# Kernel tuning notes

Hardware: AMD Instinct MI355X
Metric: run time of the kernel (lower is better)

The kernel has to match this reference:

```python
import jax, jax.numpy as jnp
import numpy as np

NUM_HEADS = 8
SCALE = 25.0
SIM_THRESH = 0.75


def setup_inputs() -> dict:
    key = jax.random.key(0)
    k1, k2, k3, k4 = jax.random.split(key, 4)
    B, N, C = 1, 2048, 1024
    x_cls = jax.random.normal(k1, (B, N, C), jnp.float32)
    cls_score = jax.random.uniform(k2, (N,), jnp.float32)
    fg_score = jax.random.uniform(k3, (N,), jnp.float32)
    W_qkv = jax.random.normal(k4, (3 * C, C), jnp.float32) * 0.02
    return {"x_cls": x_cls, "cls_score": cls_score, "fg_score": fg_score, "W_qkv": W_qkv}


def reference(x_cls, cls_score, fg_score, W_qkv):
    B, N, C = x_cls.shape
    H = NUM_HEADS
    hd = C // H
    # qkv projection (Linear without bias): [B,N,3C] -> [3,B,H,N,hd]
    qkv = (x_cls @ W_qkv.T).reshape(B, N, 3, H, hd).transpose(2, 0, 3, 1, 4)
    q, k, v = qkv[0], qkv[1], qkv[2]
    # cosine normalization
    qn = q / jnp.linalg.norm(q, axis=-1, keepdims=True)
    kn = k / jnp.linalg.norm(k, axis=-1, keepdims=True)
    vn = v / jnp.linalg.norm(v, axis=-1, keepdims=True)
    # cls_score broadcast to [1,1,1,N] (columns); fg_score is unused downstream
    cs = cls_score.reshape(1, 1, 1, N)
    # raw v-v similarity map [B,H,N,N]
    attn_cls_raw = vn @ jnp.swapaxes(vn, -2, -1)
    # use_mask=True path: mask[i,j] = cls_score[j] > cls_score[i] - 0.1
    cs_mask = (cs > jnp.swapaxes(cs, -2, -1) - 0.1).astype(x_cls.dtype)
    # scaled, score-weighted, masked attention; dropout p=0 is identity
    attn = jax.nn.softmax((qn @ jnp.swapaxes(kn, -2, -1)) * SCALE * cs * cs_mask, axis=-1)
    x = jnp.swapaxes(attn @ v, 1, 2).reshape(B, N, C)
    x_ori = jnp.swapaxes(v, 1, 2).reshape(B, N, C)
    x_out = jnp.concatenate([x, x_ori], axis=-1)  # [B,N,2C]
    # ave=True branch: head-averaged similarity + second softmax, masked renorm
    sim_raw = attn_cls_raw.sum(axis=1)[0] / H  # [N,N]
    sim_mask = (sim_raw > SIM_THRESH).astype(x_cls.dtype)
    sim_attn = attn.sum(axis=1)[0] / H
    sim_round2 = jax.nn.softmax(sim_attn, axis=-1)
    masked = sim_mask * sim_round2
    sim_round2 = masked / jnp.sum(masked, axis=-1, keepdims=True)
    return (x_out, sim_round2)
```

## Files before the change

kernel.cpp:

```cpp
#include <hip/hip_runtime.h>
#include <cstdint>

typedef unsigned short u16;
typedef __attribute__((ext_vector_type(8))) short short8;
typedef __attribute__((ext_vector_type(4))) short short4v;
typedef __attribute__((ext_vector_type(4))) float f32x4;

#define NTOK 2048
#define CDIM 1024
#define C3   3072
#define NH   8
#define HD   128

__device__ __forceinline__ float bf2f(u16 u) {
    return __uint_as_float(((unsigned)u) << 16);
}
__device__ __forceinline__ u16 f2bf(float f) {
    unsigned u = __float_as_uint(f);
    u += 0x7fffu + ((u >> 16) & 1u);
    return (u16)(u >> 16);
}
__device__ __forceinline__ void gld_lds16(const u16* g, u16* l) {
    __builtin_amdgcn_global_load_lds(
        (__attribute__((address_space(1))) void*)(u16*)g,
        (__attribute__((address_space(3))) void*)l, 16, 0, 0);
}

__global__ __launch_bounds__(256) void k_cast(const float* __restrict__ x,
                                              const float* __restrict__ w,
                                              u16* __restrict__ xb,
                                              u16* __restrict__ wb) {
    int t = blockIdx.x * blockDim.x + threadIdx.x;
    int stride = gridDim.x * blockDim.x;
    for (int i = t; i < (NTOK * CDIM) / 4; i += stride) {
        float4 v = ((const float4*)x)[i];
        ushort4 o;
        o.x = f2bf(v.x); o.y = f2bf(v.y); o.z = f2bf(v.z); o.w = f2bf(v.w);
        ((ushort4*)xb)[i] = o;
    }
    for (int i = t; i < (C3 * CDIM) / 4; i += stride) {
        float4 v = ((const float4*)w)[i];
        ushort4 o;
        o.x = f2bf(v.x); o.y = f2bf(v.y); o.z = f2bf(v.z); o.w = f2bf(v.w);
        ((ushort4*)wb)[i] = o;
    }
}

__global__ __launch_bounds__(256) void k_qkvn(const u16* __restrict__ A,
                                              const u16* __restrict__ B,
                                              u16* __restrict__ Qn,
                                              u16* __restrict__ Kn,
                                              u16* __restrict__ Vn,
                                              u16* __restrict__ Vt,
                                              float* __restrict__ out) {
    __shared__ u16 SB[2][16384];
    __shared__ float rowssq[128][2];
    u16* T = (u16*)SB;
    const int tid = threadIdx.x;
    const int lane = tid & 63;
    const int wid = tid >> 6;
    const int wm = wid >> 1, wn = wid & 1;
    const int q = lane >> 4, l16 = lane & 15;
    const int s = blockIdx.x;
    const int which = s >> 3, h = s & 7;
    const int m0 = blockIdx.y * 128, n0 = s * 128;

    const u16* aP[4];
    const u16* bP[4];
#pragma unroll
    for (int t = 0; t < 4; t++) {
        int sl = tid + t * 256;
        int r = sl >> 3, c = (sl & 7) * 8;
        aP[t] = &A[(long long)(m0 + r) * CDIM + c];
        bP[t] = &B[(long long)(n0 + r) * CDIM + c];
    }
#pragma unroll
    for (int t = 0; t < 4; t++) {
        int sl = tid + t * 256;
        gld_lds16(aP[t], &SB[0][sl * 8]);
        gld_lds16(bP[t], &SB[0][8192 + sl * 8]);
        aP[t] += 64;
        bP[t] += 64;
    }

    f32x4 zero4 = {0.f, 0.f, 0.f, 0.f};
    f32x4 acc[4][4];
#pragma unroll
    for (int i = 0; i < 4; i++)
#pragma unroll
        for (int j = 0; j < 4; j++) acc[i][j] = zero4;

    for (int jt = 0; jt < 16; ++jt) {
        const u16* As = SB[jt & 1];
        const u16* Bs = SB[jt & 1] + 8192;
        asm volatile("s_waitcnt vmcnt(0)" ::: "memory");
        __builtin_amdgcn_s_barrier();
        asm volatile("" ::: "memory");
        if (jt < 15) {
            u16* Sx = SB[(jt + 1) & 1];
#pragma unroll
            for (int t = 0; t < 4; t++) {
                int sl = tid + t * 256;
                gld_lds16(aP[t], &Sx[sl * 8]);
                gld_lds16(bP[t], &Sx[8192 + sl * 8]);
                aP[t] += 64;
                bP[t] += 64;
            }
        }
#pragma unroll
        for (int ks = 0; ks < 2; ks++) {
            short8 af[4], bfr[4];
#pragma unroll
            for (int tm = 0; tm < 4; tm++)
                af[tm] = *(const short8*)&As[(wm * 64 + tm * 16 + l16) * 64 + ks * 32 + q * 8];
#pragma unroll
            for (int tn = 0; tn < 4; tn++)
                bfr[tn] = *(const short8*)&Bs[(wn * 64 + tn * 16 + l16) * 64 + ks * 32 + q * 8];
#pragma unroll
            for (int tm = 0; tm < 4; tm++)
#pragma unroll
                for (int tn = 0; tn < 4; tn++)
                    acc[tm][tn] = __builtin_amdgcn_mfma_f32_16x16x32_bf16(
                        af[tm], bfr[tn], acc[tm][tn], 0, 0, 0);
        }
    }

    __syncthreads();
#pragma unroll
    for (int tm = 0; tm < 4; tm++)
#pragma unroll
        for (int r = 0; r < 4; r++) {
            float p = 0.f;
#pragma unroll
            for (int tn = 0; tn < 4; tn++) p += acc[tm][tn][r] * acc[tm][tn][r];
            p += __shfl_xor(p, 1);
            p += __shfl_xor(p, 2);
            p += __shfl_xor(p, 4);
            p += __shfl_xor(p, 8);
            if (l16 == 0) rowssq[wm * 64 + tm * 16 + q * 4 + r][wn] = p;
        }
    __syncthreads();
    float rinv[4][4];
#pragma unroll
    for (int tm = 0; tm < 4; tm++)
#pragma unroll
        for (int r = 0; r < 4; r++) {
            int rl = wm * 64 + tm * 16 + q * 4 + r;
            rinv[tm][r] = rsqrtf(rowssq[rl][0] + rowssq[rl][1]);
        }
    u16* dstBase = (which == 0 ? Qn : which == 1 ? Kn : Vn);
#pragma unroll
    for (int tm = 0; tm < 4; tm++)
#pragma unroll
        for (int tn = 0; tn < 4; tn++)
#pragma unroll
            for (int r = 0; r < 4; r++) {
                int rl = wm * 64 + tm * 16 + q * 4 + r;
                int d = wn * 64 + tn * 16 + l16;
                dstBase[(long long)(m0 + rl) * CDIM + h * HD + d] =
                    f2bf(acc[tm][tn][r] * rinv[tm][r]);
            }
    if (which == 2) {
#pragma unroll
        for (int tm = 0; tm < 4; tm++)
#pragma unroll
            for (int tn = 0; tn < 4; tn++)
#pragma unroll
                for (int r = 0; r < 4; r++) {
                    int rl = wm * 64 + tm * 16 + q * 4 + r;
                    int d = wn * 64 + tn * 16 + l16;
                    float v = acc[tm][tn][r];
                    out[(long long)(m0 + rl) * 2048 + 1024 + h * HD + d] = v;
                    T[rl * 136 + d] = f2bf(v);
                }
        __syncthreads();
#pragma unroll
        for (int p = 0; p < 2; p++) {
            int drow = p * 64 + (tid >> 2);
            int nc = (tid & 3) * 32;
            u16 buf[32];
#pragma unroll
            for (int i = 0; i < 32; i++) buf[i] = T[(nc + i) * 136 + drow];
            u16* dst = &Vt[(long long)(h * HD + drow) * NTOK + m0 + nc];
            *(short8*)&dst[0] = *(short8*)&buf[0];
            *(short8*)&dst[8] = *(short8*)&buf[8];
            *(short8*)&dst[16] = *(short8*)&buf[16];
            *(short8*)&dst[24] = *(short8*)&buf[24];
        }
    }
}

__global__ __launch_bounds__(256) void k_gemm_mask(const u16* __restrict__ A,
                                                   const u16* __restrict__ B,
                                                   unsigned char* __restrict__ Cv,
                                                   int K, int lda, int ldb, int ldc,
                                                   float scale) {
    __shared__ u16 As2[2][8192];
    __shared__ u16 Bs2[2][4096];
    __shared__ __attribute__((aligned(16))) unsigned char Tm[128][80];
    const int tid = threadIdx.x;
    const int lane = tid & 63;
    const int wid = tid >> 6;
    const int wm = wid >> 1, wn = wid & 1;
    const int q = lane >> 4, l16 = lane & 15;
    const int bid = blockIdx.x + 32 * blockIdx.y;
    const int sw = (bid & 7) * 64 + (bid >> 3);
    const int m0 = (sw >> 5) * 128, n0 = (sw & 31) * 64;

    const u16* aP[4];
    const u16* bP[2];
#pragma unroll
    for (int t = 0; t < 4; t++) {
        int s = tid + t * 256;
        aP[t] = &A[(long long)(m0 + (s >> 3)) * lda + (s & 7) * 8];
    }
#pragma unroll
    for (int t = 0; t < 2; t++) {
        int s = tid + t * 256;
        bP[t] = &B[(long long)(n0 + (s >> 3)) * ldb + (s & 7) * 8];
    }
#pragma unroll
    for (int t = 0; t < 4; t++) { gld_lds16(aP[t], &As2[0][(tid + t * 256) * 8]); aP[t] += 64; }
#pragma unroll
    for (int t = 0; t < 2; t++) { gld_lds16(bP[t], &Bs2[0][(tid + t * 256) * 8]); bP[t] += 64; }

    f32x4 zero4 = {0.f, 0.f, 0.f, 0.f};
    f32x4 acc[4][2];
#pragma unroll
    for (int i = 0; i < 4; i++)
#pragma unroll
        for (int j = 0; j < 2; j++) acc[i][j] = zero4;

    const int NIT = K / 64;
    for (int jt = 0; jt < NIT; ++jt) {
        const u16* As = As2[jt & 1];
        const u16* Bs = Bs2[jt & 1];
        asm volatile("s_waitcnt vmcnt(0)" ::: "memory");
        __builtin_amdgcn_s_barrier();
        asm volatile("" ::: "memory");
        if (jt < NIT - 1) {
            u16* Ax = As2[(jt + 1) & 1];
            u16* Bx = Bs2[(jt + 1) & 1];
#pragma unroll
            for (int t = 0; t < 4; t++) { gld_lds16(aP[t], &Ax[(tid + t * 256) * 8]); aP[t] += 64; }
#pragma unroll
            for (int t = 0; t < 2; t++) { gld_lds16(bP[t], &Bx[(tid + t * 256) * 8]); bP[t] += 64; }
        }
#pragma unroll
        for (int ks = 0; ks < 2; ks++) {
            short8 af[4], bfr[2];
#pragma unroll
            for (int tm = 0; tm < 4; tm++)
                af[tm] = *(const short8*)&As[(wm * 64 + tm * 16 + l16) * 64 + ks * 32 + q * 8];
#pragma unroll
            for (int tn = 0; tn < 2; tn++)
                bfr[tn] = *(const short8*)&Bs[(wn * 32 + tn * 16 + l16) * 64 + ks * 32 + q * 8];
#pragma unroll
            for (int tm = 0; tm < 4; tm++)
#pragma unroll
                for (int tn = 0; tn < 2; tn++)
                    acc[tm][tn] = __builtin_amdgcn_mfma_f32_16x16x32_bf16(
                        af[tm], bfr[tn], acc[tm][tn], 0, 0, 0);
        }
    }

#pragma unroll
    for (int tm = 0; tm < 4; tm++)
#pragma unroll
        for (int tn = 0; tn < 2; tn++) {
            int col = wn * 32 + tn * 16 + l16;
            int rowbase = wm * 64 + tm * 16 + q * 4;
#pragma unroll
            for (int r = 0; r < 4; r++)
                Tm[rowbase + r][col] = (acc[tm][tn][r] * scale > 0.75f) ? 1 : 0;
        }
    __syncthreads();
    {
        int row = tid >> 1, half = (tid & 1) * 32;
        const short8* sm = (const short8*)&Tm[row][half];
        short8* dm = (short8*)&Cv[(long long)(m0 + row) * ldc + n0 + half];
        dm[0] = sm[0]; dm[1] = sm[1];
    }
}

__global__ __launch_bounds__(256, 2) void k_attn9(const u16* __restrict__ Qn,
                                                  const u16* __restrict__ Kn,
                                                  const u16* __restrict__ Vt,
                                                  const float* __restrict__ cls,
                                                  u16* __restrict__ P,
                                                  float* __restrict__ Spart,
                                                  u16* __restrict__ Xpart) {
    __shared__ u16 Kf[2][8192];
    __shared__ u16 Vf[2][8192];
    __shared__ u16 Et[8192];
    const int bid = blockIdx.x + 16 * (blockIdx.y + 4 * blockIdx.z);
    const int sw = (bid & 7) * 64 + (bid >> 3);
    const int h = sw >> 6;
    const int jc = (sw >> 4) & 3;
    const int i0 = (sw & 15) * 128;
    const int jbase = jc * 512;
    const int tid = threadIdx.x, lane = tid & 63, wid = tid >> 6;
    const int q = lane >> 4, l16 = lane & 15;
    const int wm = wid >> 1, wn = wid & 1;

    short8 af[4][4];
#pragma unroll
    for (int m = 0; m < 4; m++)
#pragma unroll
        for (int kt = 0; kt < 4; kt++)
            af[m][kt] = *(const short8*)&Qn[(long long)(i0 + wm * 64 + m * 16 + l16) * CDIM +
                                            h * HD + kt * 32 + q * 8];
    float cls_i[4][4];
#pragma unroll
    for (int m = 0; m < 4; m++)
#pragma unroll
        for (int r = 0; r < 4; r++)
            cls_i[m][r] = cls[i0 + wm * 64 + m * 16 + q * 4 + r] - 0.1f;

    const u16* ksrc[4];
    const u16* vsrc[4];
#pragma unroll
    for (int t = 0; t < 4; t++) {
        int g = wid * 4 + t;
        int tn = g >> 2, kt = g & 3;
        ksrc[t] = &Kn[(long long)(jbase + tn * 16 + l16) * CDIM + h * HD + kt * 32 + q * 8];
        int n = g >> 1, ks = g & 1;
        vsrc[t] = &Vt[(long long)(h * HD + n * 16 + l16) * NTOK + jbase + (ks * 4 + q) * 8];
    }

    f32x4 zero4 = {0.f, 0.f, 0.f, 0.f};
    f32x4 pv[4][4];
#pragma unroll
    for (int m = 0; m < 4; m++)
#pragma unroll
        for (int n = 0; n < 4; n++) pv[m][n] = zero4;
    float sums[4][4];
#pragma unroll
    for (int m = 0; m < 4; m++)
#pragma unroll
        for (int r = 0; r < 4; r++) sums[m][r] = 0.f;

#pragma unroll
    for (int t = 0; t < 4; t++) {
        int g = wid * 4 + t;
        gld_lds16(ksrc[t], &Kf[0][(g * 64 + lane) * 8]);
        gld_lds16(vsrc[t], &Vf[0][(g * 64 + lane) * 8]);
        ksrc[t] += 64 * CDIM;
        vsrc[t] += 64;
    }

    for (int jt = 0; jt < 8; ++jt) {
        const int j0 = jbase + jt * 64;
        const int cur = jt & 1;
        u16* Kc = Kf[cur];
        if (jt == 0)
            asm volatile("s_waitcnt vmcnt(0)" ::: "memory");
        else
            asm volatile("s_waitcnt vmcnt(4)" ::: "memory");
        float cjv[2];
        cjv[0] = cls[j0 + (wn * 2 + 0) * 16 + l16];
        cjv[1] = cls[j0 + (wn * 2 + 1) * 16 + l16];
        asm volatile("" ::: "memory");
        __builtin_amdgcn_s_barrier();
        asm volatile("" ::: "memory");
        if (jt < 7) {
            u16* Kx = Kf[cur ^ 1];
            u16* Vx = Vf[cur ^ 1];
#pragma unroll
            for (int t = 0; t < 4; t++) {
                int g = wid * 4 + t;
                gld_lds16(ksrc[t], &Kx[(g * 64 + lane) * 8]);
                gld_lds16(vsrc[t], &Vx[(g * 64 + lane) * 8]);
                ksrc[t] += 64 * CDIM;
                vsrc[t] += 64;
            }
        }
#pragma unroll
        for (int tn = 0; tn < 2; tn++) {
            int tng = wn * 2 + tn;
            short8 bfr[4];
#pragma unroll
            for (int kt = 0; kt < 4; kt++)
                bfr[kt] = *(const short8*)&Kc[((tng * 4 + kt) * 64 + lane) * 8];
            float cj = cjv[tn];
            float sc = 25.f * cj;
#pragma unroll
            for (int m = 0; m < 4; m++) {
                f32x4 acc = zero4;
                __builtin_amdgcn_s_setprio(1);
#pragma unroll
                for (int kt = 0; kt < 4; kt++)
                    acc = __builtin_amdgcn_mfma_f32_16x16x32_bf16(af[m][kt], bfr[kt],
                                                                  acc, 0, 0, 0);
                __builtin_amdgcn_s_setprio(0);
                int ibase = wm * 64 + m * 16 + q * 4;
#pragma unroll
                for (int r = 0; r < 4; r++) {
                    float arg = (cj > cls_i[m][r]) ? acc[r] * sc : 0.f;
                    float e = __expf(arg);
                    sums[m][r] += e;
                    int il = ibase + r;
                    int jl = tng * 16 + l16;
                    Et[il * 64 + ((((jl >> 3) ^ (il & 7)) << 3) | (jl & 7))] = f2bf(e);
                }
            }
        }
        asm volatile("s_waitcnt lgkmcnt(0)" ::: "memory");
        __builtin_amdgcn_s_barrier();
        asm volatile("" ::: "memory");
        {
#pragma unroll
            for (int k = 0; k < 4; k++) {
                int il = k * 32 + (tid >> 3);
                int c = tid & 7;
                short8 ev = *(const short8*)&Et[il * 64 + ((c ^ (il & 7)) << 3)];
                *(short8*)&P[((long long)(h * NTOK + i0 + il)) * NTOK + j0 + c * 8] = ev;
            }
        }
        __builtin_amdgcn_s_setprio(1);
#pragma unroll
        for (int ks = 0; ks < 2; ks++) {
            short8 a2[4];
#pragma unroll
            for (int m2 = 0; m2 < 4; m2++) {
                int il = wm * 64 + m2 * 16 + l16;
                int ch = ks * 4 + q;
                a2[m2] = *(const short8*)&Et[il * 64 + ((ch ^ (il & 7)) << 3)];
            }
#pragma unroll
            for (int n2 = 0; n2 < 4; n2++) {
                short8 b2 = *(const short8*)&Vf[cur][(((wn * 4 + n2) * 2 + ks) * 64 + lane) * 8];
#pragma unroll
                for (int m2 = 0; m2 < 4; m2++)
                    pv[m2][n2] = __builtin_amdgcn_mfma_f32_16x16x32_bf16(
                        a2[m2], b2, pv[m2][n2], 0, 0, 0);
            }
        }
        __builtin_amdgcn_s_setprio(0);
    }
#pragma unroll
    for (int m = 0; m < 4; m++)
#pragma unroll
        for (int r = 0; r < 4; r++) {
            float s = sums[m][r];
            s += __shfl_xor(s, 1);
            s += __shfl_xor(s, 2);
            s += __shfl_xor(s, 4);
            s += __shfl_xor(s, 8);
            if (l16 == 0)
                Spart[((wn * 4 + jc) * NH + h) * NTOK + i0 + wm * 64 + m * 16 + q * 4 + r] = s;
        }
    u16* Xp = Xpart + (long long)jc * NTOK * CDIM;
#pragma unroll
    for (int m2 = 0; m2 < 4; m2++)
#pragma unroll
        for (int n2 = 0; n2 < 4; n2++)
#pragma unroll
            for (int r = 0; r < 4; r++) {
                int i = i0 + wm * 64 + m2 * 16 + q * 4 + r;
                int d = wn * 64 + n2 * 16 + l16;
                Xp[(long long)i * CDIM + h * HD + d] = f2bf(pv[m2][n2][r]);
            }
}

__global__ __launch_bounds__(256) void k_epi(const u16* __restrict__ Xpart,
                                             const float* __restrict__ Spart,
                                             const u16* __restrict__ P,
                                             const unsigned char* __restrict__ mask,
                                             float* __restrict__ out,
                                             float* __restrict__ out2) {
    __shared__ float redw[4];
    __shared__ float sArr[NH];
    const int i = blockIdx.x;
    const int t = threadIdx.x;
    const int lane = t & 63, w4 = t >> 6;
    if (t < NH) {
        float s = 0.f;
#pragma unroll
        for (int g = 0; g < 8; g++) s += Spart[(g * NH + t) * NTOK + i];
        sArr[t] = s;
    }
    __syncthreads();
    {
        int c = t * 4;
        int h = c >> 7;
        float acc[4] = {0.f, 0.f, 0.f, 0.f};
#pragma unroll
        for (int jc = 0; jc < 4; jc++) {
            short4v v = *(const short4v*)&Xpart[(long long)jc * NTOK * CDIM +
                                                (long long)i * CDIM + c];
#pragma unroll
            for (int k = 0; k < 4; k++) acc[k] += bf2f((u16)v[k]);
        }
        float invs = 1.f / sArr[h];
        float4 o;
        o.x = acc[0] * invs; o.y = acc[1] * invs; o.z = acc[2] * invs; o.w = acc[3] * invs;
        *(float4*)&out[(long long)i * 2048 + c] = o;
    }
    float invS[NH];
#pragma unroll
    for (int h = 0; h < NH; h++) invS[h] = 1.f / (8.f * sArr[h]);
    const int c0 = t * 8;
    float a[8] = {0.f, 0.f, 0.f, 0.f, 0.f, 0.f, 0.f, 0.f};
#pragma unroll
    for (int h = 0; h < NH; h++) {
        short8 p = *(const short8*)&P[((long long)h * NTOK + i) * NTOK + c0];
#pragma unroll
        for (int k = 0; k < 8; k++) a[k] += bf2f((u16)p[k]) * invS[h];
    }
    uint2 mv = *(const uint2*)(mask + (long long)i * NTOK + c0);
    unsigned char mk[8];
#pragma unroll
    for (int k = 0; k < 4; k++) {
        mk[k] = (unsigned char)((mv.x >> (8 * k)) & 0xffu);
        mk[k + 4] = (unsigned char)((mv.y >> (8 * k)) & 0xffu);
    }
    float e[8];
    float part = 0.f;
#pragma unroll
    for (int k = 0; k < 8; k++) {
        e[k] = __expf(a[k]);
        if (mk[k]) part += e[k];
    }
    part += __shfl_xor(part, 1);
    part += __shfl_xor(part, 2);
    part += __shfl_xor(part, 4);
    part += __shfl_xor(part, 8);
    part += __shfl_xor(part, 16);
    part += __shfl_xor(part, 32);
    if (lane == 0) redw[w4] = part;
    __syncthreads();
    float tot = (redw[0] + redw[1]) + (redw[2] + redw[3]);
    float invT = 1.f / tot;
    float o[8];
#pragma unroll
    for (int k = 0; k < 8; k++) o[k] = mk[k] ? e[k] * invT : 0.f;
    float4 o0, o1;
    o0.x = o[0]; o0.y = o[1]; o0.z = o[2]; o0.w = o[3];
    o1.x = o[4]; o1.y = o[5]; o1.z = o[6]; o1.w = o[7];
    float* dst = out2 + (long long)i * NTOK + c0;
    *(float4*)dst = o0;
    *(float4*)(dst + 4) = o1;
}

extern "C" void kernel_launch(void* const* d_in, const int* in_sizes, int n_in,
                              void* d_out, int out_size, void* d_ws,
                              size_t ws_size, hipStream_t stream) {
    (void)in_sizes; (void)n_in; (void)out_size; (void)ws_size;
    const float* x = (const float*)d_in[0];
    const float* cls = (const float*)d_in[1];
    const float* Wq = (const float*)d_in[3];
    float* out = (float*)d_out;
    char* ws = (char*)d_ws;

    u16* Xb = (u16*)(ws + 0);
    u16* Wb = (u16*)(ws + 4194304);
    u16* Xpart = (u16*)(ws + 0);
    float* Spart = (float*)(ws + 16777216);
    u16* Qn = (u16*)(ws + 23068672);
    u16* Kn = (u16*)(ws + 27262976);
    u16* Vn = (u16*)(ws + 31457280);
    u16* Vt = (u16*)(ws + 35651584);
    unsigned char* mask = (unsigned char*)(ws + 39845888);
    u16* P = (u16*)(ws + 44040192);

    k_cast<<<1024, 256, 0, stream>>>(x, Wq, Xb, Wb);

    k_qkvn<<<dim3(24, 16), 256, 0, stream>>>(Xb, Wb, Qn, Kn, Vn, Vt, out);

    k_gemm_mask<<<dim3(32, 16), 256, 0, stream>>>(
        Vn, Vn, mask, CDIM, CDIM, CDIM, NTOK, 0.125f);

    k_attn9<<<dim3(16, 4, NH), 256, 0, stream>>>(Qn, Kn, Vt, cls, P, Spart, Xpart);

    k_epi<<<NTOK, 256, 0, stream>>>(Xpart, Spart, P, mask, out,
                                    out + (long long)NTOK * 2048);
}
```

Measured before the change: 186.1 us.

## Load K and V fragments directly from global memory, double-buffer E tile

The attention kernel drops the LDS double-buffered staging of K and V tiles (global_load_lds with vmcnt waits and a barrier per iteration). MFMA B-operand fragments are now read straight from global memory for each tile, and the exp tile buffer is double-buffered in LDS. This removes one barrier per step and most of the LDS footprint, which could raise occupancy. In exchange the K/V reads are no longer prefetched, so each wave now waits on global or L2 latency. Different waves within a block also fetch overlapping data redundantly.

Result: slower. 222.8 us (+19.7%).

```diff
diff --git a/kernel.cpp b/kernel.cpp
--- a/kernel.cpp
+++ b/kernel.cpp
@@ -283,16 +283,14 @@
     }
 }
 
-__global__ __launch_bounds__(256, 2) void k_attn9(const u16* __restrict__ Qn,
-                                                  const u16* __restrict__ Kn,
-                                                  const u16* __restrict__ Vt,
-                                                  const float* __restrict__ cls,
-                                                  u16* __restrict__ P,
-                                                  float* __restrict__ Spart,
-                                                  u16* __restrict__ Xpart) {
-    __shared__ u16 Kf[2][8192];
-    __shared__ u16 Vf[2][8192];
-    __shared__ u16 Et[8192];
+__global__ __launch_bounds__(256, 2) void k_attn11(const u16* __restrict__ Qn,
+                                                   const u16* __restrict__ Kn,
+                                                   const u16* __restrict__ Vt,
+                                                   const float* __restrict__ cls,
+                                                   u16* __restrict__ P,
+                                                   float* __restrict__ Spart,
+                                                   u16* __restrict__ Xpart) {
+    __shared__ u16 Et[2][8192];
     const int bid = blockIdx.x + 16 * (blockIdx.y + 4 * blockIdx.z);
     const int sw = (bid & 7) * 64 + (bid >> 3);
     const int h = sw >> 6;
@@ -317,17 +315,6 @@
         for (int r = 0; r < 4; r++)
             cls_i[m][r] = cls[i0 + wm * 64 + m * 16 + q * 4 + r] - 0.1f;
 
-    const u16* ksrc[4];
-    const u16* vsrc[4];
-#pragma unroll
-    for (int t = 0; t < 4; t++) {
-        int g = wid * 4 + t;
-        int tn = g >> 2, kt = g & 3;
-        ksrc[t] = &Kn[(long long)(jbase + tn * 16 + l16) * CDIM + h * HD + kt * 32 + q * 8];
-        int n = g >> 1, ks = g & 1;
-        vsrc[t] = &Vt[(long long)(h * HD + n * 16 + l16) * NTOK + jbase + (ks * 4 + q) * 8];
-    }
-
     f32x4 zero4 = {0.f, 0.f, 0.f, 0.f};
     f32x4 pv[4][4];
 #pragma unroll
@@ -340,48 +327,20 @@
 #pragma unroll
         for (int r = 0; r < 4; r++) sums[m][r] = 0.f;
 
-#pragma unroll
-    for (int t = 0; t < 4; t++) {
-        int g = wid * 4 + t;
-        gld_lds16(ksrc[t], &Kf[0][(g * 64 + lane) * 8]);
-        gld_lds16(vsrc[t], &Vf[0][(g * 64 + lane) * 8]);
-        ksrc[t] += 64 * CDIM;
-        vsrc[t] += 64;
-    }
-
     for (int jt = 0; jt < 8; ++jt) {
         const int j0 = jbase + jt * 64;
-        const int cur = jt & 1;
-        u16* Kc = Kf[cur];
-        if (jt == 0)
-            asm volatile("s_waitcnt vmcnt(0)" ::: "memory");
-        else
-            asm volatile("s_waitcnt vmcnt(4)" ::: "memory");
+        u16* Ec = Et[jt & 1];
         float cjv[2];
         cjv[0] = cls[j0 + (wn * 2 + 0) * 16 + l16];
         cjv[1] = cls[j0 + (wn * 2 + 1) * 16 + l16];
-        asm volatile("" ::: "memory");
-        __builtin_amdgcn_s_barrier();
-        asm volatile("" ::: "memory");
-        if (jt < 7) {
-            u16* Kx = Kf[cur ^ 1];
-            u16* Vx = Vf[cur ^ 1];
-#pragma unroll
-            for (int t = 0; t < 4; t++) {
-                int g = wid * 4 + t;
-                gld_lds16(ksrc[t], &Kx[(g * 64 + lane) * 8]);
-                gld_lds16(vsrc[t], &Vx[(g * 64 + lane) * 8]);
-                ksrc[t] += 64 * CDIM;
-                vsrc[t] += 64;
-            }
-        }
 #pragma unroll
         for (int tn = 0; tn < 2; tn++) {
             int tng = wn * 2 + tn;
             short8 bfr[4];
 #pragma unroll
             for (int kt = 0; kt < 4; kt++)
-                bfr[kt] = *(const short8*)&Kc[((tng * 4 + kt) * 64 + lane) * 8];
+                bfr[kt] = *(const short8*)&Kn[(long long)(j0 + tng * 16 + l16) * CDIM +
+                                              h * HD + kt * 32 + q * 8];
             float cj = cjv[tn];
             float sc = 25.f * cj;
 #pragma unroll
@@ -401,7 +360,7 @@
                     sums[m][r] += e;
                     int il = ibase + r;
                     int jl = tng * 16 + l16;
-                    Et[il * 64 + ((((jl >> 3) ^ (il & 7)) << 3) | (jl & 7))] = f2bf(e);
+                    Ec[il * 64 + ((((jl >> 3) ^ (il & 7)) << 3) | (jl & 7))] = f2bf(e);
                 }
             }
         }
@@ -413,7 +372,7 @@
             for (int k = 0; k < 4; k++) {
                 int il = k * 32 + (tid >> 3);
                 int c = tid & 7;
-                short8 ev = *(const short8*)&Et[il * 64 + ((c ^ (il & 7)) << 3)];
+                short8 ev = *(const short8*)&Ec[il * 64 + ((c ^ (il & 7)) << 3)];
                 *(short8*)&P[((long long)(h * NTOK + i0 + il)) * NTOK + j0 + c * 8] = ev;
             }
         }
@@ -425,11 +384,12 @@
             for (int m2 = 0; m2 < 4; m2++) {
                 int il = wm * 64 + m2 * 16 + l16;
                 int ch = ks * 4 + q;
-                a2[m2] = *(const short8*)&Et[il * 64 + ((ch ^ (il & 7)) << 3)];
+                a2[m2] = *(const short8*)&Ec[il * 64 + ((ch ^ (il & 7)) << 3)];
             }
 #pragma unroll
             for (int n2 = 0; n2 < 4; n2++) {
-                short8 b2 = *(const short8*)&Vf[cur][(((wn * 4 + n2) * 2 + ks) * 64 + lane) * 8];
+                short8 b2 = *(const short8*)&Vt[(long long)(h * HD + (wn * 4 + n2) * 16 + l16) * NTOK +
+                                                j0 + (ks * 4 + q) * 8];
 #pragma unroll
                 for (int m2 = 0; m2 < 4; m2++)
                     pv[m2][n2] = __builtin_amdgcn_mfma_f32_16x16x32_bf16(
@@ -571,7 +531,7 @@
     k_gemm_mask<<<dim3(32, 16), 256, 0, stream>>>(
         Vn, Vn, mask, CDIM, CDIM, CDIM, NTOK, 0.125f);
 
-    k_attn9<<<dim3(16, 4, NH), 256, 0, stream>>>(Qn, Kn, Vt, cls, P, Spart, Xpart);
+    k_attn11<<<dim3(16, 4, NH), 256, 0, stream>>>(Qn, Kn, Vt, cls, P, Spart, Xpart);
 
     k_epi<<<NTOK, 256, 0, stream>>>(Xpart, Spart, P, mask, out,
                                     out + (long long)NTOK * 2048);
```
